# Optimization experiments

Hardware: AMD Instinct MI355X
Metric: run time of the kernel (lower is better)

Reference implementation:

```python
import jax, jax.numpy as jnp
import numpy as np

RES = 64
FDIM = 32
NMOD = 3
HID = 64
NCLS = 4
NFREQ = 6
IN_DIM = FDIM * NMOD + 3 * (2 * NFREQ + 1)  # 135


def trilinear_sample(grid, pts):
    """Torch F.grid_sample(mode='bilinear', padding_mode='zeros', align_corners=True).
    grid: [C, D, H, W]; pts: [M, 3] with (x, y, z) in [-1, 1], x indexes W, y->H, z->D.
    Returns [M, C]."""
    C, D, H, W = grid.shape
    x, y, z = pts[:, 0], pts[:, 1], pts[:, 2]
    ix = (x + 1.0) * 0.5 * (W - 1)
    iy = (y + 1.0) * 0.5 * (H - 1)
    iz = (z + 1.0) * 0.5 * (D - 1)
    ix0 = jnp.floor(ix); iy0 = jnp.floor(iy); iz0 = jnp.floor(iz)
    fx = ix - ix0; fy = iy - iy0; fz = iz - iz0
    ix0i = ix0.astype(jnp.int32); ix1i = ix0i + 1
    iy0i = iy0.astype(jnp.int32); iy1i = iy0i + 1
    iz0i = iz0.astype(jnp.int32); iz1i = iz0i + 1

    def corner(zc, yc, xc, w):
        valid = ((zc >= 0) & (zc < D) & (yc >= 0) & (yc < H) & (xc >= 0) & (xc < W))
        zcc = jnp.clip(zc, 0, D - 1)
        ycc = jnp.clip(yc, 0, H - 1)
        xcc = jnp.clip(xc, 0, W - 1)
        v = grid[:, zcc, ycc, xcc]  # [C, M]
        return v * (w * valid.astype(grid.dtype))

    wx0 = 1.0 - fx; wx1 = fx
    wy0 = 1.0 - fy; wy1 = fy
    wz0 = 1.0 - fz; wz1 = fz
    out = (corner(iz0i, iy0i, ix0i, wz0 * wy0 * wx0)
           + corner(iz0i, iy0i, ix1i, wz0 * wy0 * wx1)
           + corner(iz0i, iy1i, ix0i, wz0 * wy1 * wx0)
           + corner(iz0i, iy1i, ix1i, wz0 * wy1 * wx1)
           + corner(iz1i, iy0i, ix0i, wz1 * wy0 * wx0)
           + corner(iz1i, iy0i, ix1i, wz1 * wy0 * wx1)
           + corner(iz1i, iy1i, ix0i, wz1 * wy1 * wx0)
           + corner(iz1i, iy1i, ix1i, wz1 * wy1 * wx1))
    return out.T  # [M, C]


def positional_encoding(x):
    # gamma(p) = [p, sin(2^0 pi p), cos(2^0 pi p), ..., sin(2^(L-1) pi p), cos(2^(L-1) pi p)]
    freqs = 2.0 ** jnp.arange(NFREQ, dtype=x.dtype)  # [L]
    enc = [x]
    for i in range(NFREQ):
        a = jnp.pi * freqs[i] * x
        enc.append(jnp.sin(a))
        enc.append(jnp.cos(a))
    return jnp.concatenate(enc, axis=-1)  # [..., 3*(2L+1)]


def setup_inputs() -> dict:
    key = jax.random.key(0)
    ks = jax.random.split(key, 8)
    B, N = 4, 131072
    points = jax.random.uniform(ks[0], (B, N, 3), jnp.float32, -1.0, 1.0)
    grids = jax.random.normal(ks[1], (NMOD, FDIM, RES, RES, RES), jnp.float32) * 0.1

    def xavier(k, fan_in, fan_out):
        a = np.sqrt(6.0 / (fan_in + fan_out))
        return jax.random.uniform(k, (fan_in, fan_out), jnp.float32, -a, a)

    W0 = xavier(ks[2], IN_DIM, HID); b0 = jnp.zeros((HID,), jnp.float32)
    W1 = xavier(ks[3], HID, HID); b1 = jnp.zeros((HID,), jnp.float32)
    W2 = xavier(ks[4], HID, 1 + NCLS); b2 = jnp.zeros((1 + NCLS,), jnp.float32)
    return {"points": points, "grids": grids, "W0": W0, "b0": b0,
            "W1": W1, "b1": b1, "W2": W2, "b2": b2}


def reference(points, grids, W0, b0, W1, b1, W2, b2):
    B, N, _ = points.shape
    pts = points.reshape(B * N, 3)
    # fuse all 3 modalities: cat along feature dim, modality-major order
    feats = jax.vmap(lambda g: trilinear_sample(g, pts))(grids)  # [3, M, C]
    fused = jnp.transpose(feats, (1, 0, 2)).reshape(B * N, NMOD * FDIM)
    pe = positional_encoding(pts)  # [M, 39]
    h = jnp.concatenate([fused, pe], axis=-1)  # [M, 135]
    h = jax.nn.relu(h @ W0 + b0)
    h = jax.nn.relu(h @ W1 + b1)
    o = h @ W2 + b2  # [M, 1 + num_classes]
    density = jax.nn.softplus(o[..., 0]).reshape(B, N)
    seg_logits = o[..., 1:].reshape(B, N, NCLS)
    return density, seg_logits
```

## Files before the change

### kernel.cpp

```cpp
#include <hip/hip_runtime.h>
#include <hip/hip_bf16.h>
#include <math.h>

#define RESX 64
#define NVOX (RESX * RESX * RESX)
#define FDIM 32
#define NMOD 3
#define HID 64
#define NCLS 4
#define NFREQ 6
#define INDIM 135
#define TPB 64
#define XK 168
#define XSTR 65
#define MSTRIDE_U (NVOX * FDIM / 2)
#define NCELL 4096
#define NREP 16
#define TRB (NMOD * (NVOX / 64))
#define HISTB 2048
#define PACKB 15

typedef short bf16x8 __attribute__((ext_vector_type(8)));
typedef float f32x4  __attribute__((ext_vector_type(4)));

static __device__ __forceinline__ float ubf_lo(unsigned int u) {
    return __uint_as_float(u << 16);
}
static __device__ __forceinline__ float ubf_hi(unsigned int u) {
    return __uint_as_float(u & 0xFFFF0000u);
}
static __device__ __forceinline__ unsigned int pack_bf16(float lo, float hi) {
    float2 f2; f2.x = lo; f2.y = hi;
    __hip_bfloat162 h = __float22bfloat162_rn(f2);
    return *reinterpret_cast<unsigned int*>(&h);
}

static __device__ __forceinline__ int cell_of_point(const float* __restrict__ points, int i) {
    const float px = points[i * 3 + 0];
    const float py = points[i * 3 + 1];
    const float pz = points[i * 3 + 2];
    int x0 = (int)floorf((px + 1.0f) * 0.5f * (RESX - 1));
    int y0 = (int)floorf((py + 1.0f) * 0.5f * (RESX - 1));
    int z0 = (int)floorf((pz + 1.0f) * 0.5f * (RESX - 1));
    x0 = min(max(x0, 0), RESX - 1);
    y0 = min(max(y0, 0), RESX - 1);
    z0 = min(max(z0, 0), RESX - 1);
    return ((z0 >> 2) << 8) | ((y0 >> 2) << 4) | (x0 >> 2);
}

#define W0PACK (5 * 4 * 64 * 8)
#define W1PACK (2 * 4 * 64 * 8)
#define W2PACK (2 * 64 * 8)

__global__ void pre_kernel(const float* __restrict__ g,
                           __hip_bfloat16* __restrict__ gt,
                           const float* __restrict__ W0,
                           const float* __restrict__ W1,
                           const float* __restrict__ W2,
                           __hip_bfloat16* __restrict__ wb,
                           const float* __restrict__ points,
                           unsigned int* __restrict__ hist, int M) {
    __shared__ float tile[FDIM][65];
    const int bid = blockIdx.x;
    const int t   = threadIdx.x;
    if (bid < TRB) {
        const int m  = bid >> 12;
        const int v0 = (bid & 4095) << 6;
#pragma unroll
        for (int pass = 0; pass < 8; ++pass) {
            const int c = pass * 4 + (t >> 6);
            const int v = t & 63;
            tile[c][v] = g[(size_t)(m * FDIM + c) * NVOX + v0 + v];
        }
        __syncthreads();
        unsigned int* gtu = reinterpret_cast<unsigned int*>(gt);
#pragma unroll
        for (int pass = 0; pass < 4; ++pass) {
            const int flat = pass * 256 + t;
            const int v  = flat >> 4;
            const int cu = flat & 15;
            gtu[(size_t)(m * NVOX + v0 + v) * 16 + cu] =
                pack_bf16(tile[2 * cu][v], tile[2 * cu + 1][v]);
        }
    } else if (bid < TRB + HISTB) {
        const int hb = bid - TRB;
        const int i  = hb * 256 + t;
        const int r  = hb & (NREP - 1);
        if (i < M) atomicAdd(&hist[r * NCELL + cell_of_point(points, i)], 1u);
    } else {
        const int tt = (bid - TRB - HISTB) * 256 + t;
        const int NT = PACKB * 256;
        for (int idx = tt; idx < W0PACK; idx += NT) {
            const int j = idx & 7, l = (idx >> 3) & 63, nt = (idx >> 9) & 3, s = idx >> 11;
            const int k = 32 * s + (l >> 4) * 8 + j;
            const int o = 16 * nt + (l & 15);
            const float v = (k < INDIM) ? W0[k * HID + o] : 0.0f;
            wb[idx] = __float2bfloat16(v);
        }
        for (int idx = tt; idx < W1PACK; idx += NT) {
            const int j = idx & 7, l = (idx >> 3) & 63, nt = (idx >> 9) & 3, s = idx >> 11;
            const int k = 32 * s + (l >> 4) * 8 + j;
            const int o = 16 * nt + (l & 15);
            wb[W0PACK + idx] = __float2bfloat16(W1[k * HID + o]);
        }
        for (int idx = tt; idx < W2PACK; idx += NT) {
            const int j = idx & 7, l = (idx >> 3) & 63, s = idx >> 9;
            const int k = 32 * s + (l >> 4) * 8 + j;
            const int o = l & 15;
            wb[W0PACK + W1PACK + idx] =
                __float2bfloat16((o < NCLS + 1) ? W2[k * (NCLS + 1) + o] : 0.0f);
        }
    }
}

__global__ void scan_rep_kernel(unsigned int* __restrict__ hist,
                                unsigned int* __restrict__ tot) {
    const int c = blockIdx.x * 256 + threadIdx.x;
    unsigned int run = 0;
#pragma unroll
    for (int r = 0; r < NREP; ++r) {
        const unsigned int v = hist[r * NCELL + c];
        hist[r * NCELL + c] = run;
        run += v;
    }
    tot[c] = run;
}

__global__ __launch_bounds__(1024) void scan_kernel(const unsigned int* __restrict__ tot,
                                                    unsigned int* __restrict__ cbase) {
    __shared__ unsigned int s[1024];
    const int t = threadIdx.x;
    unsigned int v[4];
#pragma unroll
    for (int j = 0; j < 4; ++j) v[j] = tot[4 * t + j];
    const unsigned int sum = v[0] + v[1] + v[2] + v[3];
    s[t] = sum;
    __syncthreads();
    for (int off = 1; off < 1024; off <<= 1) {
        const unsigned int x = (t >= off) ? s[t - off] : 0u;
        __syncthreads();
        s[t] += x;
        __syncthreads();
    }
    unsigned int excl = s[t] - sum;
#pragma unroll
    for (int j = 0; j < 4; ++j) { cbase[4 * t + j] = excl; excl += v[j]; }
}

__global__ void scatter_kernel(const float* __restrict__ points,
                               const unsigned int* __restrict__ cbase,
                               unsigned int* __restrict__ hist,
                               unsigned int* __restrict__ perm, int M) {
    const int i = blockIdx.x * 256 + threadIdx.x;
    if (i < M) {
        const int c = cell_of_point(points, i);
        const int r = blockIdx.x & (NREP - 1);
        const unsigned int pos = cbase[c] + atomicAdd(&hist[r * NCELL + c], 1u);
        perm[pos] = (unsigned int)i;
    }
}

template <bool SORT>
__global__ __launch_bounds__(256, 6) void fused_mfma_kernel(
    const float* __restrict__ points,
    const __hip_bfloat16* __restrict__ gt,
    const __hip_bfloat16* __restrict__ wb,
    const unsigned int* __restrict__ perm,
    const float* __restrict__ b0, const float* __restrict__ b1,
    const float* __restrict__ b2,
    float* __restrict__ density, float* __restrict__ seg) {
    __shared__ __align__(16) __hip_bfloat16 Xs[TPB * XK];
    __shared__ __align__(16) int4   PB[TPB];
    __shared__ __align__(16) float4 PW[TPB];
    __shared__ __align__(16) float4 PXI[TPB];
    __shared__ int PIdx[TPB];
    const int tid = threadIdx.x;
    const int chunk = gridDim.x >> 3;
    const int sbid  = (blockIdx.x & 7) * chunk + (blockIdx.x >> 3);
    const int p0    = sbid * TPB;

    const int l = tid & 63;
    const int w = __builtin_amdgcn_readfirstlane(tid >> 6);

    if (l < 16) {
        const int p  = w * 16 + l;
        const int sp = p0 + p;
        const int gp = SORT ? (int)perm[sp] : sp;
        const float px = points[gp * 3 + 0];
        const float py = points[gp * 3 + 1];
        const float pz = points[gp * 3 + 2];
        const float ix = (px + 1.0f) * 0.5f * (RESX - 1);
        const float iy = (py + 1.0f) * 0.5f * (RESX - 1);
        const float iz = (pz + 1.0f) * 0.5f * (RESX - 1);
        const float fx0 = floorf(ix), fy0 = floorf(iy), fz0 = floorf(iz);
        const float fx = ix - fx0, fy = iy - fy0, fz = iz - fz0;
        int x0 = (int)fx0, y0 = (int)fy0, z0 = (int)fz0;
        x0 = min(max(x0, 0), RESX - 1);
        y0 = min(max(y0, 0), RESX - 1);
        z0 = min(max(z0, 0), RESX - 1);
        const int y1 = min(y0 + 1, RESX - 1);
        const int z1 = min(z0 + 1, RESX - 1);
        const float wy0 = 1.0f - fy, wy1 = fy;
        const float wz0 = 1.0f - fz, wz1 = fz;
        PB[p] = make_int4((z0 * 4096 + y0 * 64 + x0) * 16,
                          (z0 * 4096 + y1 * 64 + x0) * 16,
                          (z1 * 4096 + y0 * 64 + x0) * 16,
                          (z1 * 4096 + y1 * 64 + x0) * 16);
        PW[p]  = make_float4(wz0 * wy0, wz0 * wy1, wz1 * wy0, wz1 * wy1);
        PXI[p] = make_float4(px, py, pz, fx);
        PIdx[p] = gp;
    }

    {
        const int hw   = tid >> 5;
        const int lane = tid & 31;
        const int half = lane >> 4;
        const int lc   = lane & 15;
        const unsigned int* gtu = reinterpret_cast<const unsigned int*>(gt) + lane;
#pragma unroll
        for (int i = 0; i < 8; ++i) {
            const int p = hw * 8 + i;
            const int4   bq = PB[p];
            const float4 wq = PW[p];
            const float  fx = PXI[p].w;
            const float wxh = half ? fx : 1.0f - fx;
            const float w00 = wq.x * wxh, w01 = wq.y * wxh;
            const float w10 = wq.z * wxh, w11 = wq.w * wxh;
            float alo[NMOD], ahi[NMOD];
#pragma unroll
            for (int m = 0; m < NMOD; ++m) {
                const unsigned int* gm = gtu + m * MSTRIDE_U;
                const unsigned int u0 = gm[bq.x];
                const unsigned int u1 = gm[bq.y];
                const unsigned int u2 = gm[bq.z];
                const unsigned int u3 = gm[bq.w];
                float lo, hi;
                lo = w00 * ubf_lo(u0);              hi = w00 * ubf_hi(u0);
                lo = fmaf(w01, ubf_lo(u1), lo);     hi = fmaf(w01, ubf_hi(u1), hi);
                lo = fmaf(w10, ubf_lo(u2), lo);     hi = fmaf(w10, ubf_hi(u2), hi);
                lo = fmaf(w11, ubf_lo(u3), lo);     hi = fmaf(w11, ubf_hi(u3), hi);
                alo[m] = lo; ahi[m] = hi;
            }
#pragma unroll
            for (int m = 0; m < NMOD; ++m) {
                const float lo = alo[m] + __shfl_xor(alo[m], 16, 64);
                const float hi = ahi[m] + __shfl_xor(ahi[m], 16, 64);
                if (lane < 16) {
                    *reinterpret_cast<unsigned int*>(&Xs[p * XK + m * FDIM + 2 * lc]) =
                        pack_bf16(lo, hi);
                }
            }
        }
    }

    {
        const int pt  = w * 16 + (l & 15);
        const int gq2 = l >> 4;
        const float4 pxi = PXI[pt];
        const float c3[3] = {pxi.x, pxi.y, pxi.z};
        __hip_bfloat16* xr = &Xs[pt * XK];
        if (gq2 == 3) {
            xr[96] = __float2bfloat16(c3[0]);
            xr[97] = __float2bfloat16(c3[1]);
            xr[98] = __float2bfloat16(c3[2]);
            xr[135] = __float2bfloat16(0.0f);
        }
        if (gq2 == 2) {
            unsigned int* xz = reinterpret_cast<unsigned int*>(&xr[136]);
#pragma unroll
            for (int k = 0; k < 12; ++k) xz[k] = 0u;
        }
        {
            const int f = gq2;
            const float hf = 0.5f * (float)(1 << f);
#pragma unroll
            for (int d = 0; d < 3; ++d) {
                const float r  = c3[d] * hf;
                const float rf = r - floorf(r);
                xr[99 + 6 * f + d]     = __float2bfloat16(__builtin_amdgcn_sinf(rf));
                xr[99 + 6 * f + 3 + d] = __float2bfloat16(__builtin_amdgcn_cosf(rf));
            }
        }
        if (gq2 < 2) {
            const int f = gq2 + 4;
            const float hf = 0.5f * (float)(1 << f);
#pragma unroll
            for (int d = 0; d < 3; ++d) {
                const float r  = c3[d] * hf;
                const float rf = r - floorf(r);
                xr[99 + 6 * f + d]     = __float2bfloat16(__builtin_amdgcn_sinf(rf));
                xr[99 + 6 * f + 3 + d] = __float2bfloat16(__builtin_amdgcn_cosf(rf));
            }
        }
    }

    const int col = l & 15;
    const int g   = l >> 4;

    f32x4 acc0[4];
#pragma unroll
    for (int nt = 0; nt < 4; ++nt) {
        const float bv = b0[nt * 16 + col];
        acc0[nt] = (f32x4){bv, bv, bv, bv};
    }
    {
        const __hip_bfloat16* arow = &Xs[(w * 16 + col) * XK];
#pragma unroll
        for (int s = 0; s < 5; ++s) {
            const bf16x8 af = *reinterpret_cast<const bf16x8*>(arow + s * 32 + g * 8);
#pragma unroll
            for (int nt = 0; nt < 4; ++nt) {
                const bf16x8 bfr = *reinterpret_cast<const bf16x8*>(wb + (size_t)((s * 4 + nt) * 64 + l) * 8);
                acc0[nt] = __builtin_amdgcn_mfma_f32_16x16x32_bf16(af, bfr, acc0[nt], 0, 0, 0);
            }
        }
    }
#pragma unroll
    for (int nt = 0; nt < 4; ++nt)
#pragma unroll
        for (int r = 0; r < 4; ++r) {
            const float v = fmaxf(acc0[nt][r], 0.0f);
            Xs[(w * 16 + g * 4 + r) * XK + 96 + nt * 16 + col] = __float2bfloat16(v);
        }

    f32x4 acc1[4];
#pragma unroll
    for (int nt = 0; nt < 4; ++nt) {
        const float bv = b1[nt * 16 + col];
        acc1[nt] = (f32x4){bv, bv, bv, bv};
    }
    {
        const __hip_bfloat16* arow = &Xs[(w * 16 + col) * XK + 96];
        const __hip_bfloat16* wb1  = wb + W0PACK;
#pragma unroll
        for (int s = 0; s < 2; ++s) {
            const bf16x8 af = *reinterpret_cast<const bf16x8*>(arow + s * 32 + g * 8);
#pragma unroll
            for (int nt = 0; nt < 4; ++nt) {
                const bf16x8 bfr = *reinterpret_cast<const bf16x8*>(wb1 + (size_t)((s * 4 + nt) * 64 + l) * 8);
                acc1[nt] = __builtin_amdgcn_mfma_f32_16x16x32_bf16(af, bfr, acc1[nt], 0, 0, 0);
            }
        }
    }
#pragma unroll
    for (int nt = 0; nt < 4; ++nt)
#pragma unroll
        for (int r = 0; r < 4; ++r) {
            const float v = fmaxf(acc1[nt][r], 0.0f);
            Xs[(w * 16 + g * 4 + r) * XK + nt * 16 + col] = __float2bfloat16(v);
        }

    f32x4 acc2;
    {
        const float bv = (col < NCLS + 1) ? b2[col] : 0.0f;
        acc2 = (f32x4){bv, bv, bv, bv};
        const __hip_bfloat16* arow = &Xs[(w * 16 + col) * XK];
        const __hip_bfloat16* wb2  = wb + W0PACK + W1PACK;
#pragma unroll
        for (int s = 0; s < 2; ++s) {
            const bf16x8 af  = *reinterpret_cast<const bf16x8*>(arow + s * 32 + g * 8);
            const bf16x8 bfr = *reinterpret_cast<const bf16x8*>(wb2 + (size_t)(s * 64 + l) * 8);
            acc2 = __builtin_amdgcn_mfma_f32_16x16x32_bf16(af, bfr, acc2, 0, 0, 0);
        }
    }
    if (col < NCLS + 1) {
        float* osr = reinterpret_cast<float*>(&Xs[0]);
#pragma unroll
        for (int r = 0; r < 4; ++r) {
            const int row = w * 16 + g * 4 + r;
            osr[(row * XK + 128) / 2 + col] = acc2[r];
        }
    }

    if (l < 16) {
        const int row = w * 16 + l;
        const int gp2 = PIdx[row];
        const float* osr = reinterpret_cast<const float*>(&Xs[0]) + (row * XK + 128) / 2;
        const float4 o0123 = *reinterpret_cast<const float4*>(osr);
        const float o4 = osr[4];
        const float e  = __builtin_amdgcn_exp2f(fabsf(o0123.x) * -1.44269504f);
        const float sp = fmaxf(o0123.x, 0.0f) + 0.69314718f * __builtin_amdgcn_logf(1.0f + e);
        density[gp2] = sp;
        reinterpret_cast<float4*>(seg)[gp2] = make_float4(o0123.y, o0123.z, o0123.w, o4);
    }
}

__global__ __launch_bounds__(256, 4) void fused_nerf_fallback(
    const float* __restrict__ points,
    const float* __restrict__ grids,
    const float* __restrict__ W0, const float* __restrict__ b0,
    const float* __restrict__ W1, const float* __restrict__ b1,
    const float* __restrict__ W2, const float* __restrict__ b2,
    float* __restrict__ density, float* __restrict__ seg) {
    __shared__ float xT[INDIM + 1][XSTR];
    const int tid = threadIdx.x;
    const int p0  = blockIdx.x * TPB;
    {
        const int hw   = tid >> 5;
        const int lane = tid & 31;
        for (int i = 0; i < TPB / 8; ++i) {
            const int p  = hw * (TPB / 8) + i;
            const int gp = p0 + p;
            const float px = points[gp * 3 + 0];
            const float py = points[gp * 3 + 1];
            const float pz = points[gp * 3 + 2];
            const float ix = (px + 1.0f) * 0.5f * (RESX - 1);
            const float iy = (py + 1.0f) * 0.5f * (RESX - 1);
            const float iz = (pz + 1.0f) * 0.5f * (RESX - 1);
            const float fx0 = floorf(ix), fy0 = floorf(iy), fz0 = floorf(iz);
            const float fx = ix - fx0, fy = iy - fy0, fz = iz - fz0;
            int ix0 = (int)fx0, iy0 = (int)fy0, iz0 = (int)fz0;
            ix0 = min(max(ix0, 0), RESX - 1);
            iy0 = min(max(iy0, 0), RESX - 1);
            iz0 = min(max(iz0, 0), RESX - 1);
            const int ix1 = min(ix0 + 1, RESX - 1);
            const int iy1 = min(iy0 + 1, RESX - 1);
            const int iz1 = min(iz0 + 1, RESX - 1);
            const float wx1 = fx, wx0 = 1.0f - fx;
            const float wy1 = fy, wy0 = 1.0f - fy;
            const float wz1 = fz, wz0 = 1.0f - fz;
            const int vz0 = iz0 * 4096, vz1 = iz1 * 4096;
            const int vy0 = iy0 * 64,   vy1 = iy1 * 64;
            const int v000 = vz0 + vy0 + ix0, v001 = vz0 + vy0 + ix1;
            const int v010 = vz0 + vy1 + ix0, v011 = vz0 + vy1 + ix1;
            const int v100 = vz1 + vy0 + ix0, v101 = vz1 + vy0 + ix1;
            const int v110 = vz1 + vy1 + ix0, v111 = vz1 + vy1 + ix1;
            const float w000 = wz0 * wy0 * wx0, w001 = wz0 * wy0 * wx1;
            const float w010 = wz0 * wy1 * wx0, w011 = wz0 * wy1 * wx1;
            const float w100 = wz1 * wy0 * wx0, w101 = wz1 * wy0 * wx1;
            const float w110 = wz1 * wy1 * wx0, w111 = wz1 * wy1 * wx1;
#pragma unroll
            for (int m = 0; m < NMOD; ++m) {
                const float* gb = grids + (size_t)(m * FDIM + lane) * NVOX;
                float acc;
                acc = w000 * gb[v000];
                acc = fmaf(w001, gb[v001], acc);
                acc = fmaf(w010, gb[v010], acc);
                acc = fmaf(w011, gb[v011], acc);
                acc = fmaf(w100, gb[v100], acc);
                acc = fmaf(w101, gb[v101], acc);
                acc = fmaf(w110, gb[v110], acc);
                acc = fmaf(w111, gb[v111], acc);
                xT[m * FDIM + lane][p] = acc;
            }
        }
    }
    {
        const int p  = tid & 63;
        const int gq = tid >> 6;
        const int gp = p0 + p;
        float c3[3];
        c3[0] = points[gp * 3 + 0];
        c3[1] = points[gp * 3 + 1];
        c3[2] = points[gp * 3 + 2];
        if (gq == 3) {
#pragma unroll
            for (int d = 0; d < 3; ++d) xT[96 + d][p] = c3[d];
        }
#pragma unroll
        for (int f = 0; f < NFREQ; ++f) {
            if ((f & 3) != gq) continue;
            const float fr = (float)(1 << f);
#pragma unroll
            for (int d = 0; d < 3; ++d) {
                const float a = 3.14159274101257324f * fr * c3[d];
                xT[99 + 6 * f + d][p]     = sinf(a);
                xT[99 + 6 * f + 3 + d][p] = cosf(a);
            }
        }
    }
    __syncthreads();
    const int pl = tid & 63;
    const int wv = __builtin_amdgcn_readfirstlane(tid >> 6);
    const int gp = p0 + pl;
    float acc[16];
#pragma unroll
    for (int j = 0; j < 16; ++j) acc[j] = b0[wv * 16 + j];
    for (int k = 0; k < INDIM; ++k) {
        const float xk = xT[k][pl];
        const float* wr = W0 + k * HID + wv * 16;
#pragma unroll
        for (int j = 0; j < 16; ++j) acc[j] = fmaf(xk, wr[j], acc[j]);
    }
#pragma unroll
    for (int j = 0; j < 16; ++j) acc[j] = fmaxf(acc[j], 0.0f);
    __syncthreads();
#pragma unroll
    for (int j = 0; j < 16; ++j) xT[wv * 16 + j][pl] = acc[j];
    __syncthreads();
    float acc1[16];
#pragma unroll
    for (int j = 0; j < 16; ++j) acc1[j] = b1[wv * 16 + j];
    for (int k = 0; k < HID; ++k) {
        const float xk = xT[k][pl];
        const float* wr = W1 + k * HID + wv * 16;
#pragma unroll
        for (int j = 0; j < 16; ++j) acc1[j] = fmaf(xk, wr[j], acc1[j]);
    }
#pragma unroll
    for (int j = 0; j < 16; ++j) acc1[j] = fmaxf(acc1[j], 0.0f);
    __syncthreads();
#pragma unroll
    for (int j = 0; j < 16; ++j) xT[wv * 16 + j][pl] = acc1[j];
    __syncthreads();
    if (wv == 0) {
        float o[5];
#pragma unroll
        for (int j = 0; j < 5; ++j) o[j] = b2[j];
        for (int k = 0; k < HID; ++k) {
            const float xk = xT[k][pl];
            const float* wr = W2 + k * (1 + NCLS);
#pragma unroll
            for (int j = 0; j < 5; ++j) o[j] = fmaf(xk, wr[j], o[j]);
        }
        const float d = fmaxf(o[0], 0.0f) + log1pf(expf(-fabsf(o[0])));
        density[gp] = d;
        reinterpret_cast<float4*>(seg)[gp] = make_float4(o[1], o[2], o[3], o[4]);
    }
}

extern "C" void kernel_launch(void* const* d_in, const int* in_sizes, int n_in,
                              void* d_out, int out_size, void* d_ws, size_t ws_size,
                              hipStream_t stream) {
    const float* points = (const float*)d_in[0];
    const float* grids  = (const float*)d_in[1];
    const float* W0     = (const float*)d_in[2];
    const float* b0     = (const float*)d_in[3];
    const float* W1     = (const float*)d_in[4];
    const float* b1     = (const float*)d_in[5];
    const float* W2     = (const float*)d_in[6];
    const float* b2     = (const float*)d_in[7];

    const int M = in_sizes[0] / 3;
    float* density = (float*)d_out;
    float* seg     = density + M;

    const size_t gt_b   = (size_t)NMOD * NVOX * FDIM * sizeof(__hip_bfloat16);
    const size_t wb_b   = 32768;
    const size_t hist_b = (size_t)NREP * NCELL * sizeof(unsigned int);
    const size_t tot_b  = NCELL * sizeof(unsigned int);
    const size_t cb_b   = NCELL * sizeof(unsigned int);
    const size_t perm_b = (size_t)M * sizeof(unsigned int);
    const int nblk = M / TPB;

    if (ws_size >= gt_b + wb_b + hist_b + tot_b + cb_b + perm_b) {
        char* p = (char*)d_ws;
        __hip_bfloat16* gt    = (__hip_bfloat16*)p;  p += gt_b;
        __hip_bfloat16* wbp   = (__hip_bfloat16*)p;  p += wb_b;
        unsigned int*   hist  = (unsigned int*)p;    p += hist_b;
        unsigned int*   tot   = (unsigned int*)p;    p += tot_b;
        unsigned int*   cbase = (unsigned int*)p;    p += cb_b;
        unsigned int*   perm  = (unsigned int*)p;

        hipMemsetAsync(hist, 0, hist_b, stream);
        pre_kernel<<<TRB + HISTB + PACKB, 256, 0, stream>>>(
            grids, gt, W0, W1, W2, wbp, points, hist, M);
        scan_rep_kernel<<<NCELL / 256, 256, 0, stream>>>(hist, tot);
        scan_kernel<<<1, 1024, 0, stream>>>(tot, cbase);
        scatter_kernel<<<(M + 255) / 256, 256, 0, stream>>>(points, cbase, hist, perm, M);
        fused_mfma_kernel<true><<<nblk, 256, 0, stream>>>(
            points, gt, wbp, perm, b0, b1, b2, density, seg);
    } else if (ws_size >= gt_b + wb_b) {
        char* p = (char*)d_ws;
        __hip_bfloat16* gt  = (__hip_bfloat16*)p;  p += gt_b;
        __hip_bfloat16* wbp = (__hip_bfloat16*)p;
        pre_kernel<<<TRB + PACKB, 256, 0, stream>>>(
            grids, gt, W0, W1, W2, wbp, points, (unsigned int*)nullptr, 0);
        fused_mfma_kernel<false><<<nblk, 256, 0, stream>>>(
            points, gt, wbp, (const unsigned int*)nullptr, b0, b1, b2, density, seg);
    } else {
        fused_nerf_fallback<<<nblk, 256, 0, stream>>>(
            points, grids, W0, b0, W1, b1, W2, b2, density, seg);
    }
}
```

Baseline: 157.7 us.

## Switch grid and MLP to fp16 with packed half2 interpolation, merge scans, scatter points

Stores the transposed feature grid and packed weights in fp16 instead of bf16. Trilinear interpolation now runs in packed half2 FMAs, and the MLP uses f16 MFMA. The two scan kernels are merged into one kernel that writes absolute offsets back into the histogram. The scatter now writes sorted float4 points (xyz plus original index), so the main kernel no longer does an indirect gather through perm. This cuts ALU work, launches and dependent loads, at the cost of fp16 range and precision in the accumulation.

After: 155.8 us. About the same (-1.2%).

```diff
diff --git a/kernel.cpp b/kernel.cpp
--- a/kernel.cpp
+++ b/kernel.cpp
@@ -1,5 +1,6 @@
 #include <hip/hip_runtime.h>
 #include <hip/hip_bf16.h>
+#include <hip/hip_fp16.h>
 #include <math.h>
 
 #define RESX 64
@@ -13,35 +14,28 @@
 #define TPB 64
 #define XK 168
 #define XSTR 65
-#define MSTRIDE_U (NVOX * FDIM / 2)
+#define MSTRIDE_B (NVOX * FDIM * 2)
 #define NCELL 4096
 #define NREP 16
 #define TRB (NMOD * (NVOX / 64))
 #define HISTB 2048
 #define PACKB 15
 
-typedef short bf16x8 __attribute__((ext_vector_type(8)));
-typedef float f32x4  __attribute__((ext_vector_type(4)));
-
-static __device__ __forceinline__ float ubf_lo(unsigned int u) {
-    return __uint_as_float(u << 16);
-}
-static __device__ __forceinline__ float ubf_hi(unsigned int u) {
-    return __uint_as_float(u & 0xFFFF0000u);
-}
-static __device__ __forceinline__ unsigned int pack_bf16(float lo, float hi) {
-    float2 f2; f2.x = lo; f2.y = hi;
-    __hip_bfloat162 h = __float22bfloat162_rn(f2);
-    return *reinterpret_cast<unsigned int*>(&h);
-}
-
-static __device__ __forceinline__ int cell_of_point(const float* __restrict__ points, int i) {
-    const float px = points[i * 3 + 0];
-    const float py = points[i * 3 + 1];
-    const float pz = points[i * 3 + 2];
-    int x0 = (int)floorf((px + 1.0f) * 0.5f * (RESX - 1));
-    int y0 = (int)floorf((py + 1.0f) * 0.5f * (RESX - 1));
-    int z0 = (int)floorf((pz + 1.0f) * 0.5f * (RESX - 1));
+typedef _Float16 f16x8 __attribute__((ext_vector_type(8)));
+typedef float    f32x4 __attribute__((ext_vector_type(4)));
+
+static __device__ __forceinline__ __half2 u2h(unsigned int u) {
+    return __builtin_bit_cast(__half2, u);
+}
+static __device__ __forceinline__ unsigned int h2u(__half2 h) {
+    return __builtin_bit_cast(unsigned int, h);
+}
+
+static __device__ __forceinline__ int cell_coords(float px, float py, float pz,
+                                                  int& x0, int& y0, int& z0) {
+    x0 = (int)floorf((px + 1.0f) * 0.5f * (RESX - 1));
+    y0 = (int)floorf((py + 1.0f) * 0.5f * (RESX - 1));
+    z0 = (int)floorf((pz + 1.0f) * 0.5f * (RESX - 1));
     x0 = min(max(x0, 0), RESX - 1);
     y0 = min(max(y0, 0), RESX - 1);
     z0 = min(max(z0, 0), RESX - 1);
@@ -53,11 +47,11 @@
 #define W2PACK (2 * 64 * 8)
 
 __global__ void pre_kernel(const float* __restrict__ g,
-                           __hip_bfloat16* __restrict__ gt,
+                           _Float16* __restrict__ gt,
                            const float* __restrict__ W0,
                            const float* __restrict__ W1,
                            const float* __restrict__ W2,
-                           __hip_bfloat16* __restrict__ wb,
+                           _Float16* __restrict__ wb,
                            const float* __restrict__ points,
                            unsigned int* __restrict__ hist, int M) {
     __shared__ float tile[FDIM][65];
@@ -80,13 +74,18 @@
             const int v  = flat >> 4;
             const int cu = flat & 15;
             gtu[(size_t)(m * NVOX + v0 + v) * 16 + cu] =
-                pack_bf16(tile[2 * cu][v], tile[2 * cu + 1][v]);
+                h2u(__floats2half2_rn(tile[2 * cu][v], tile[2 * cu + 1][v]));
         }
     } else if (bid < TRB + HISTB) {
         const int hb = bid - TRB;
         const int i  = hb * 256 + t;
         const int r  = hb & (NREP - 1);
-        if (i < M) atomicAdd(&hist[r * NCELL + cell_of_point(points, i)], 1u);
+        if (i < M) {
+            int x0, y0, z0;
+            const int c = cell_coords(points[i * 3], points[i * 3 + 1], points[i * 3 + 2],
+                                      x0, y0, z0);
+            atomicAdd(&hist[r * NCELL + c], 1u);
+        }
     } else {
         const int tt = (bid - TRB - HISTB) * 256 + t;
         const int NT = PACKB * 256;
@@ -94,46 +93,41 @@
             const int j = idx & 7, l = (idx >> 3) & 63, nt = (idx >> 9) & 3, s = idx >> 11;
             const int k = 32 * s + (l >> 4) * 8 + j;
             const int o = 16 * nt + (l & 15);
-            const float v = (k < INDIM) ? W0[k * HID + o] : 0.0f;
-            wb[idx] = __float2bfloat16(v);
+            wb[idx] = (_Float16)((k < INDIM) ? W0[k * HID + o] : 0.0f);
         }
         for (int idx = tt; idx < W1PACK; idx += NT) {
             const int j = idx & 7, l = (idx >> 3) & 63, nt = (idx >> 9) & 3, s = idx >> 11;
             const int k = 32 * s + (l >> 4) * 8 + j;
             const int o = 16 * nt + (l & 15);
-            wb[W0PACK + idx] = __float2bfloat16(W1[k * HID + o]);
+            wb[W0PACK + idx] = (_Float16)W1[k * HID + o];
         }
         for (int idx = tt; idx < W2PACK; idx += NT) {
             const int j = idx & 7, l = (idx >> 3) & 63, s = idx >> 9;
             const int k = 32 * s + (l >> 4) * 8 + j;
             const int o = l & 15;
             wb[W0PACK + W1PACK + idx] =
-                __float2bfloat16((o < NCLS + 1) ? W2[k * (NCLS + 1) + o] : 0.0f);
-        }
-    }
-}
-
-__global__ void scan_rep_kernel(unsigned int* __restrict__ hist,
-                                unsigned int* __restrict__ tot) {
-    const int c = blockIdx.x * 256 + threadIdx.x;
-    unsigned int run = 0;
-#pragma unroll
-    for (int r = 0; r < NREP; ++r) {
-        const unsigned int v = hist[r * NCELL + c];
-        hist[r * NCELL + c] = run;
-        run += v;
-    }
-    tot[c] = run;
-}
-
-__global__ __launch_bounds__(1024) void scan_kernel(const unsigned int* __restrict__ tot,
-                                                    unsigned int* __restrict__ cbase) {
+                (_Float16)((o < NCLS + 1) ? W2[k * (NCLS + 1) + o] : 0.0f);
+        }
+    }
+}
+
+__global__ __launch_bounds__(1024) void scan_fuse_kernel(unsigned int* __restrict__ hist) {
     __shared__ unsigned int s[1024];
     const int t = threadIdx.x;
-    unsigned int v[4];
-#pragma unroll
-    for (int j = 0; j < 4; ++j) v[j] = tot[4 * t + j];
-    const unsigned int sum = v[0] + v[1] + v[2] + v[3];
+    unsigned int tot[4];
+#pragma unroll
+    for (int j = 0; j < 4; ++j) {
+        const int c = 4 * t + j;
+        unsigned int run = 0;
+#pragma unroll
+        for (int r = 0; r < NREP; ++r) {
+            const unsigned int v = hist[r * NCELL + c];
+            hist[r * NCELL + c] = run;
+            run += v;
+        }
+        tot[j] = run;
+    }
+    const unsigned int sum = tot[0] + tot[1] + tot[2] + tot[3];
     s[t] = sum;
     __syncthreads();
     for (int off = 1; off < 1024; off <<= 1) {
@@ -142,34 +136,40 @@
         s[t] += x;
         __syncthreads();
     }
-    unsigned int excl = s[t] - sum;
-#pragma unroll
-    for (int j = 0; j < 4; ++j) { cbase[4 * t + j] = excl; excl += v[j]; }
+    unsigned int cb = s[t] - sum;
+#pragma unroll
+    for (int j = 0; j < 4; ++j) {
+        const int c = 4 * t + j;
+#pragma unroll
+        for (int r = 0; r < NREP; ++r) hist[r * NCELL + c] += cb;
+        cb += tot[j];
+    }
 }
 
 __global__ void scatter_kernel(const float* __restrict__ points,
-                               const unsigned int* __restrict__ cbase,
                                unsigned int* __restrict__ hist,
-                               unsigned int* __restrict__ perm, int M) {
+                               float4* __restrict__ pts4, int M) {
     const int i = blockIdx.x * 256 + threadIdx.x;
     if (i < M) {
-        const int c = cell_of_point(points, i);
+        const float px = points[i * 3], py = points[i * 3 + 1], pz = points[i * 3 + 2];
+        int x0, y0, z0;
+        const int c = cell_coords(px, py, pz, x0, y0, z0);
         const int r = blockIdx.x & (NREP - 1);
-        const unsigned int pos = cbase[c] + atomicAdd(&hist[r * NCELL + c], 1u);
-        perm[pos] = (unsigned int)i;
+        const unsigned int pos = atomicAdd(&hist[r * NCELL + c], 1u);
+        pts4[pos] = make_float4(px, py, pz, __int_as_float(i));
     }
 }
 
 template <bool SORT>
 __global__ __launch_bounds__(256, 6) void fused_mfma_kernel(
     const float* __restrict__ points,
-    const __hip_bfloat16* __restrict__ gt,
-    const __hip_bfloat16* __restrict__ wb,
-    const unsigned int* __restrict__ perm,
+    const float4* __restrict__ pts4,
+    const _Float16* __restrict__ gt,
+    const _Float16* __restrict__ wb,
     const float* __restrict__ b0, const float* __restrict__ b1,
     const float* __restrict__ b2,
     float* __restrict__ density, float* __restrict__ seg) {
-    __shared__ __align__(16) __hip_bfloat16 Xs[TPB * XK];
+    __shared__ __align__(16) _Float16 Xs[TPB * XK];
     __shared__ __align__(16) int4   PB[TPB];
     __shared__ __align__(16) float4 PW[TPB];
     __shared__ __align__(16) float4 PXI[TPB];
@@ -185,10 +185,14 @@
     if (l < 16) {
         const int p  = w * 16 + l;
         const int sp = p0 + p;
-        const int gp = SORT ? (int)perm[sp] : sp;
-        const float px = points[gp * 3 + 0];
-        const float py = points[gp * 3 + 1];
-        const float pz = points[gp * 3 + 2];
+        float px, py, pz; int gp;
+        if (SORT) {
+            const float4 q = pts4[sp];
+            px = q.x; py = q.y; pz = q.z; gp = __float_as_int(q.w);
+        } else {
+            px = points[sp * 3]; py = points[sp * 3 + 1]; pz = points[sp * 3 + 2];
+            gp = sp;
+        }
         const float ix = (px + 1.0f) * 0.5f * (RESX - 1);
         const float iy = (py + 1.0f) * 0.5f * (RESX - 1);
         const float iz = (pz + 1.0f) * 0.5f * (RESX - 1);
@@ -202,10 +206,10 @@
         const int z1 = min(z0 + 1, RESX - 1);
         const float wy0 = 1.0f - fy, wy1 = fy;
         const float wz0 = 1.0f - fz, wz1 = fz;
-        PB[p] = make_int4((z0 * 4096 + y0 * 64 + x0) * 16,
-                          (z0 * 4096 + y1 * 64 + x0) * 16,
-                          (z1 * 4096 + y0 * 64 + x0) * 16,
-                          (z1 * 4096 + y1 * 64 + x0) * 16);
+        PB[p] = make_int4((z0 * 4096 + y0 * 64 + x0) * 64,
+                          (z0 * 4096 + y1 * 64 + x0) * 64,
+                          (z1 * 4096 + y0 * 64 + x0) * 64,
+                          (z1 * 4096 + y1 * 64 + x0) * 64);
         PW[p]  = make_float4(wz0 * wy0, wz0 * wy1, wz1 * wy0, wz1 * wy1);
         PXI[p] = make_float4(px, py, pz, fx);
         PIdx[p] = gp;
@@ -216,7 +220,7 @@
         const int lane = tid & 31;
         const int half = lane >> 4;
         const int lc   = lane & 15;
-        const unsigned int* gtu = reinterpret_cast<const unsigned int*>(gt) + lane;
+        const char* gbase = reinterpret_cast<const char*>(gt) + lane * 4;
 #pragma unroll
         for (int i = 0; i < 8; ++i) {
             const int p = hw * 8 + i;
@@ -224,30 +228,30 @@
             const float4 wq = PW[p];
             const float  fx = PXI[p].w;
             const float wxh = half ? fx : 1.0f - fx;
-            const float w00 = wq.x * wxh, w01 = wq.y * wxh;
-            const float w10 = wq.z * wxh, w11 = wq.w * wxh;
-            float alo[NMOD], ahi[NMOD];
+            const __half2 h00 = __float2half2_rn(wq.x * wxh);
+            const __half2 h01 = __float2half2_rn(wq.y * wxh);
+            const __half2 h10 = __float2half2_rn(wq.z * wxh);
+            const __half2 h11 = __float2half2_rn(wq.w * wxh);
+            unsigned int accu[NMOD];
 #pragma unroll
             for (int m = 0; m < NMOD; ++m) {
-                const unsigned int* gm = gtu + m * MSTRIDE_U;
-                const unsigned int u0 = gm[bq.x];
-                const unsigned int u1 = gm[bq.y];
-                const unsigned int u2 = gm[bq.z];
-                const unsigned int u3 = gm[bq.w];
-                float lo, hi;
-                lo = w00 * ubf_lo(u0);              hi = w00 * ubf_hi(u0);
-                lo = fmaf(w01, ubf_lo(u1), lo);     hi = fmaf(w01, ubf_hi(u1), hi);
-                lo = fmaf(w10, ubf_lo(u2), lo);     hi = fmaf(w10, ubf_hi(u2), hi);
-                lo = fmaf(w11, ubf_lo(u3), lo);     hi = fmaf(w11, ubf_hi(u3), hi);
-                alo[m] = lo; ahi[m] = hi;
+                const char* gm = gbase + (size_t)m * MSTRIDE_B;
+                const unsigned int u0 = *reinterpret_cast<const unsigned int*>(gm + bq.x);
+                const unsigned int u1 = *reinterpret_cast<const unsigned int*>(gm + bq.y);
+                const unsigned int u2 = *reinterpret_cast<const unsigned int*>(gm + bq.z);
+                const unsigned int u3 = *reinterpret_cast<const unsigned int*>(gm + bq.w);
+                __half2 a = __hmul2(h00, u2h(u0));
+                a = __hfma2(h01, u2h(u1), a);
+                a = __hfma2(h10, u2h(u2), a);
+                a = __hfma2(h11, u2h(u3), a);
+                accu[m] = h2u(a);
             }
 #pragma unroll
             for (int m = 0; m < NMOD; ++m) {
-                const float lo = alo[m] + __shfl_xor(alo[m], 16, 64);
-                const float hi = ahi[m] + __shfl_xor(ahi[m], 16, 64);
+                const unsigned int other = __shfl_xor(accu[m], 16, 64);
+                const __half2 sum = __hadd2(u2h(accu[m]), u2h(other));
                 if (lane < 16) {
-                    *reinterpret_cast<unsigned int*>(&Xs[p * XK + m * FDIM + 2 * lc]) =
-                        pack_bf16(lo, hi);
+                    *reinterpret_cast<unsigned int*>(&Xs[p * XK + m * FDIM + 2 * lc]) = h2u(sum);
                 }
             }
         }
@@ -258,12 +262,12 @@
         const int gq2 = l >> 4;
         const float4 pxi = PXI[pt];
         const float c3[3] = {pxi.x, pxi.y, pxi.z};
-        __hip_bfloat16* xr = &Xs[pt * XK];
+        _Float16* xr = &Xs[pt * XK];
         if (gq2 == 3) {
-            xr[96] = __float2bfloat16(c3[0]);
-            xr[97] = __float2bfloat16(c3[1]);
-            xr[98] = __float2bfloat16(c3[2]);
-            xr[135] = __float2bfloat16(0.0f);
+            xr[96]  = (_Float16)c3[0];
+            xr[97]  = (_Float16)c3[1];
+            xr[98]  = (_Float16)c3[2];
+            xr[135] = (_Float16)0.0f;
         }
         if (gq2 == 2) {
             unsigned int* xz = reinterpret_cast<unsigned int*>(&xr[136]);
@@ -277,8 +281,8 @@
             for (int d = 0; d < 3; ++d) {
                 const float r  = c3[d] * hf;
                 const float rf = r - floorf(r);
-                xr[99 + 6 * f + d]     = __float2bfloat16(__builtin_amdgcn_sinf(rf));
-                xr[99 + 6 * f + 3 + d] = __float2bfloat16(__builtin_amdgcn_cosf(rf));
+                xr[99 + 6 * f + d]     = (_Float16)__builtin_amdgcn_sinf(rf);
+                xr[99 + 6 * f + 3 + d] = (_Float16)__builtin_amdgcn_cosf(rf);
             }
         }
         if (gq2 < 2) {
@@ -288,8 +292,8 @@
             for (int d = 0; d < 3; ++d) {
                 const float r  = c3[d] * hf;
                 const float rf = r - floorf(r);
-                xr[99 + 6 * f + d]     = __float2bfloat16(__builtin_amdgcn_sinf(rf));
-                xr[99 + 6 * f + 3 + d] = __float2bfloat16(__builtin_amdgcn_cosf(rf));
+                xr[99 + 6 * f + d]     = (_Float16)__builtin_amdgcn_sinf(rf);
+                xr[99 + 6 * f + 3 + d] = (_Float16)__builtin_amdgcn_cosf(rf);
             }
         }
     }
@@ -304,14 +308,14 @@
         acc0[nt] = (f32x4){bv, bv, bv, bv};
     }
     {
-        const __hip_bfloat16* arow = &Xs[(w * 16 + col) * XK];
+        const _Float16* arow = &Xs[(w * 16 + col) * XK];
 #pragma unroll
         for (int s = 0; s < 5; ++s) {
-            const bf16x8 af = *reinterpret_cast<const bf16x8*>(arow + s * 32 + g * 8);
+            const f16x8 af = *reinterpret_cast<const f16x8*>(arow + s * 32 + g * 8);
 #pragma unroll
             for (int nt = 0; nt < 4; ++nt) {
-                const bf16x8 bfr = *reinterpret_cast<const bf16x8*>(wb + (size_t)((s * 4 + nt) * 64 + l) * 8);
-                acc0[nt] = __builtin_amdgcn_mfma_f32_16x16x32_bf16(af, bfr, acc0[nt], 0, 0, 0);
+                const f16x8 bfr = *reinterpret_cast<const f16x8*>(wb + (size_t)((s * 4 + nt) * 64 + l) * 8);
+                acc0[nt] = __builtin_amdgcn_mfma_f32_16x16x32_f16(af, bfr, acc0[nt], 0, 0, 0);
             }
         }
     }
@@ -319,8 +323,8 @@
     for (int nt = 0; nt < 4; ++nt)
 #pragma unroll
         for (int r = 0; r < 4; ++r) {
-            const float v = fmaxf(acc0[nt][r], 0.0f);
-            Xs[(w * 16 + g * 4 + r) * XK + 96 + nt * 16 + col] = __float2bfloat16(v);
+            Xs[(w * 16 + g * 4 + r) * XK + 96 + nt * 16 + col] =
+                (_Float16)fmaxf(acc0[nt][r], 0.0f);
         }
 
     f32x4 acc1[4];
@@ -330,15 +334,15 @@
         acc1[nt] = (f32x4){bv, bv, bv, bv};
     }
     {
-        const __hip_bfloat16* arow = &Xs[(w * 16 + col) * XK + 96];
-        const __hip_bfloat16* wb1  = wb + W0PACK;
+        const _Float16* arow = &Xs[(w * 16 + col) * XK + 96];
+        const _Float16* wb1  = wb + W0PACK;
 #pragma unroll
         for (int s = 0; s < 2; ++s) {
-            const bf16x8 af = *reinterpret_cast<const bf16x8*>(arow + s * 32 + g * 8);
+            const f16x8 af = *reinterpret_cast<const f16x8*>(arow + s * 32 + g * 8);
 #pragma unroll
             for (int nt = 0; nt < 4; ++nt) {
-                const bf16x8 bfr = *reinterpret_cast<const bf16x8*>(wb1 + (size_t)((s * 4 + nt) * 64 + l) * 8);
-                acc1[nt] = __builtin_amdgcn_mfma_f32_16x16x32_bf16(af, bfr, acc1[nt], 0, 0, 0);
+                const f16x8 bfr = *reinterpret_cast<const f16x8*>(wb1 + (size_t)((s * 4 + nt) * 64 + l) * 8);
+                acc1[nt] = __builtin_amdgcn_mfma_f32_16x16x32_f16(af, bfr, acc1[nt], 0, 0, 0);
             }
         }
     }
@@ -346,21 +350,21 @@
     for (int nt = 0; nt < 4; ++nt)
 #pragma unroll
         for (int r = 0; r < 4; ++r) {
-            const float v = fmaxf(acc1[nt][r], 0.0f);
-            Xs[(w * 16 + g * 4 + r) * XK + nt * 16 + col] = __float2bfloat16(v);
+            Xs[(w * 16 + g * 4 + r) * XK + nt * 16 + col] =
+                (_Float16)fmaxf(acc1[nt][r], 0.0f);
         }
 
     f32x4 acc2;
     {
         const float bv = (col < NCLS + 1) ? b2[col] : 0.0f;
         acc2 = (f32x4){bv, bv, bv, bv};
-        const __hip_bfloat16* arow = &Xs[(w * 16 + col) * XK];
-        const __hip_bfloat16* wb2  = wb + W0PACK + W1PACK;
+        const _Float16* arow = &Xs[(w * 16 + col) * XK];
+        const _Float16* wb2  = wb + W0PACK + W1PACK;
 #pragma unroll
         for (int s = 0; s < 2; ++s) {
-            const bf16x8 af  = *reinterpret_cast<const bf16x8*>(arow + s * 32 + g * 8);
-            const bf16x8 bfr = *reinterpret_cast<const bf16x8*>(wb2 + (size_t)(s * 64 + l) * 8);
-            acc2 = __builtin_amdgcn_mfma_f32_16x16x32_bf16(af, bfr, acc2, 0, 0, 0);
+            const f16x8 af  = *reinterpret_cast<const f16x8*>(arow + s * 32 + g * 8);
+            const f16x8 bfr = *reinterpret_cast<const f16x8*>(wb2 + (size_t)(s * 64 + l) * 8);
+            acc2 = __builtin_amdgcn_mfma_f32_16x16x32_f16(af, bfr, acc2, 0, 0, 0);
         }
     }
     if (col < NCLS + 1) {
@@ -535,39 +539,34 @@
     float* density = (float*)d_out;
     float* seg     = density + M;
 
-    const size_t gt_b   = (size_t)NMOD * NVOX * FDIM * sizeof(__hip_bfloat16);
+    const size_t gt_b   = (size_t)NMOD * NVOX * FDIM * sizeof(_Float16);
     const size_t wb_b   = 32768;
     const size_t hist_b = (size_t)NREP * NCELL * sizeof(unsigned int);
-    const size_t tot_b  = NCELL * sizeof(unsigned int);
-    const size_t cb_b   = NCELL * sizeof(unsigned int);
-    const size_t perm_b = (size_t)M * sizeof(unsigned int);
+    const size_t pts_b  = (size_t)M * sizeof(float4);
     const int nblk = M / TPB;
 
-    if (ws_size >= gt_b + wb_b + hist_b + tot_b + cb_b + perm_b) {
+    if (ws_size >= gt_b + wb_b + hist_b + pts_b) {
         char* p = (char*)d_ws;
-        __hip_bfloat16* gt    = (__hip_bfloat16*)p;  p += gt_b;
-        __hip_bfloat16* wbp   = (__hip_bfloat16*)p;  p += wb_b;
-        unsigned int*   hist  = (unsigned int*)p;    p += hist_b;
-        unsigned int*   tot   = (unsigned int*)p;    p += tot_b;
-        unsigned int*   cbase = (unsigned int*)p;    p += cb_b;
-        unsigned int*   perm  = (unsigned int*)p;
+        _Float16*     gt   = (_Float16*)p;      p += gt_b;
+        _Float16*     wbp  = (_Float16*)p;      p += wb_b;
+        unsigned int* hist = (unsigned int*)p;  p += hist_b;
+        float4*       pts4 = (float4*)p;
 
         hipMemsetAsync(hist, 0, hist_b, stream);
         pre_kernel<<<TRB + HISTB + PACKB, 256, 0, stream>>>(
             grids, gt, W0, W1, W2, wbp, points, hist, M);
-        scan_rep_kernel<<<NCELL / 256, 256, 0, stream>>>(hist, tot);
-        scan_kernel<<<1, 1024, 0, stream>>>(tot, cbase);
-        scatter_kernel<<<(M + 255) / 256, 256, 0, stream>>>(points, cbase, hist, perm, M);
+        scan_fuse_kernel<<<1, 1024, 0, stream>>>(hist);
+        scatter_kernel<<<(M + 255) / 256, 256, 0, stream>>>(points, hist, pts4, M);
         fused_mfma_kernel<true><<<nblk, 256, 0, stream>>>(
-            points, gt, wbp, perm, b0, b1, b2, density, seg);
+            points, pts4, gt, wbp, b0, b1, b2, density, seg);
     } else if (ws_size >= gt_b + wb_b) {
         char* p = (char*)d_ws;
-        __hip_bfloat16* gt  = (__hip_bfloat16*)p;  p += gt_b;
-        __hip_bfloat16* wbp = (__hip_bfloat16*)p;
-        pre_kernel<<<TRB + PACKB, 256, 0, stream>>>(
+        _Float16* gt  = (_Float16*)p;  p += gt_b;
+        _Float16* wbp = (_Float16*)p;
+        pre_kernel<<<TRB + HISTB + PACKB, 256, 0, stream>>>(
             grids, gt, W0, W1, W2, wbp, points, (unsigned int*)nullptr, 0);
         fused_mfma_kernel<false><<<nblk, 256, 0, stream>>>(
-            points, gt, wbp, (const unsigned int*)nullptr, b0, b1, b2, density, seg);
+            points, (const float4*)nullptr, gt, wbp, b0, b1, b2, density, seg);
     } else {
         fused_nerf_fallback<<<nblk, 256, 0, stream>>>(
             points, grids, W0, b0, W1, b1, W2, b2, density, seg);
```
